# Kernel tuning notes

Measured on AMD Instinct MI355X. Metric: run time of the kernel, lower is better.

## Reference

```python
import jax, jax.numpy as jnp
import numpy as np

N = 50000      # nodes per graph
E = 600000     # edges per graph
IN_DIM = 512
HID = 128
LAYERS = 2


def setup_inputs() -> dict:
    key = jax.random.key(0)
    ks = jax.random.split(key, 24)
    s = 0.05
    inp = {
        "src_fea": jax.random.normal(ks[0], (N, IN_DIM), jnp.float32),
        "trg_fea": jax.random.normal(ks[1], (N, IN_DIM), jnp.float32),
        "src_row": jax.random.randint(ks[2], (E,), 0, N, jnp.int32),
        "src_col": jax.random.randint(ks[3], (E,), 0, N, jnp.int32),
        "trg_row": jax.random.randint(ks[4], (E,), 0, N, jnp.int32),
        "trg_col": jax.random.randint(ks[5], (E,), 0, N, jnp.int32),
        # fx: Linear(in,hid)+GELU+Linear(hid,hid)+GELU
        "fxW1": jax.random.normal(ks[6], (IN_DIM, HID), jnp.float32) * s,
        "fxb1": jnp.zeros((HID,), jnp.float32),
        "fxW2": jax.random.normal(ks[7], (HID, HID), jnp.float32) * s,
        "fxb2": jnp.zeros((HID,), jnp.float32),
        # edge_att_mlp: Linear(2h,20)+ReLU+Linear(20,10)+ReLU+Linear(10,1)+ReLU
        "eaW1": jax.random.normal(ks[8], (2 * HID, 20), jnp.float32) * s,
        "eab1": jnp.zeros((20,), jnp.float32),
        "eaW2": jax.random.normal(ks[9], (20, 10), jnp.float32) * s,
        "eab2": jnp.zeros((10,), jnp.float32),
        "eaW3": jax.random.normal(ks[10], (10, 1), jnp.float32) * s,
        "eab3": jnp.zeros((1,), jnp.float32),
        # GraphConv (PyG-style, bias=False): out = x@Wroot + agg@Wrel
        "convWroot": jax.random.normal(ks[11], (LAYERS, HID, HID), jnp.float32) * s,
        "convWrel": jax.random.normal(ks[12], (LAYERS, HID, HID), jnp.float32) * s,
    }
    return inp


def _fx(x, W1, b1, W2, b2):
    h = jax.nn.gelu(x @ W1 + b1, approximate=False)
    return jax.nn.gelu(h @ W2 + b2, approximate=False)


def _edge_att(e, eaW1, eab1, eaW2, eab2, eaW3, eab3):
    h = jax.nn.relu(e @ eaW1 + eab1)
    h = jax.nn.relu(h @ eaW2 + eab2)
    h = jax.nn.relu(h @ eaW3 + eab3)
    return jax.nn.sigmoid(h)  # [E,1]


def _graph_conv(x, row, col, ew, Wroot, Wrel):
    # message from source (row) gathered, weighted, aggregated at target (col)
    msg = ew[:, None] * x[row]                                  # [E,h]
    agg = jax.ops.segment_sum(msg, col, num_segments=N)         # [N,h]
    return x @ Wroot + agg @ Wrel


def _branch(x0, row, col, convWroot, convWrel, eaW1, eab1, eaW2, eab2, eaW3, eab3, hard):
    xs, cfds = [], []
    x = x0
    for i in range(LAYERS):
        edge_rep = jnp.concatenate([x[row], x[col]], axis=-1)    # [E,2h]
        att = _edge_att(edge_rep, eaW1, eab1, eaW2, eab2, eaW3, eab3)[:, 0]
        wc = (att + hard) * 0.5
        wo = 1.0 - wc
        x = jax.nn.soft_sign(_graph_conv(x, row, col, wc, convWroot[i], convWrel[i]))
        cfd = jax.nn.soft_sign(_graph_conv(x, row, col, wo, convWroot[i], convWrel[i]))
        xs.append(x)
        cfds.append(cfd)
    return xs, cfds


def reference(src_fea, trg_fea, src_row, src_col, trg_row, trg_col,
              fxW1, fxb1, fxW2, fxb2,
              eaW1, eab1, eaW2, eab2, eaW3, eab3,
              convWroot, convWrel):
    src1 = _fx(src_fea, fxW1, fxb1, fxW2, fxb2)
    trg1 = _fx(trg_fea, fxW1, fxb1, fxW2, fxb2)
    ea = (eaW1, eab1, eaW2, eab2, eaW3, eab3)
    xs_s, cf_s = _branch(src1, src_row, src_col, convWroot, convWrel, *ea, 0.0)
    xs_t, cf_t = _branch(trg1, trg_row, trg_col, convWroot, convWrel, *ea, 0.0)
    # stack: [src1, xs_s..., trg1, xs_t..., cf_s..., cf_t...] -> [2+2*LAYERS+2*LAYERS? no: 10, N, h]
    return jnp.stack([src1] + xs_s + [trg1] + xs_t + cf_s + cf_t, axis=0)
```

## Files before the change

### kernel.cpp

```cpp
#include <hip/hip_runtime.h>
#include <math.h>
#include <stdint.h>


typedef __attribute__((ext_vector_type(8))) short bh8;
typedef __attribute__((ext_vector_type(4))) float f4;

__device__ __forceinline__ float relu_f(float x) { return x > 0.f ? x : 0.f; }

__device__ __forceinline__ unsigned short f2bf(float f) {
    union { float f; unsigned u; } v; v.f = f;
    unsigned r = v.u + 0x7FFF + ((v.u >> 16) & 1);
    return (unsigned short)(r >> 16);
}
__device__ __forceinline__ float bf2f(unsigned short b) {
    union { unsigned u; float f; } v; v.u = ((unsigned)b) << 16;
    return v.f;
}

template<int ACT>
__device__ __forceinline__ float act_fn(float x) {
    if (ACT == 1) return 0.5f * x * (1.f + erff(x * 0.70710678118654752f));
    if (ACT == 2) return x / (1.f + fabsf(x));
    return x;
}

__device__ __forceinline__ float edge_att_mlp(const unsigned short* p1,
                                              const unsigned short* p2,
                                              const float* w2, const float* b2s,
                                              const float* w3s, const float* sb1,
                                              float sb3)
{
    bh8 a0 = *(const bh8*)&p1[0];
    bh8 a1 = *(const bh8*)&p1[8];
    ushort4 a2 = *(const ushort4*)&p1[16];
    bh8 b0 = *(const bh8*)&p2[0];
    bh8 b1 = *(const bh8*)&p2[8];
    ushort4 b2 = *(const ushort4*)&p2[16];

    float h1[20];
    #pragma unroll
    for (int j = 0; j < 8; ++j)
        h1[j] = relu_f(bf2f((unsigned short)a0[j]) + bf2f((unsigned short)b0[j]) + sb1[j]);
    #pragma unroll
    for (int j = 0; j < 8; ++j)
        h1[8 + j] = relu_f(bf2f((unsigned short)a1[j]) + bf2f((unsigned short)b1[j]) + sb1[8 + j]);
    h1[16] = relu_f(bf2f(a2.x) + bf2f(b2.x) + sb1[16]);
    h1[17] = relu_f(bf2f(a2.y) + bf2f(b2.y) + sb1[17]);
    h1[18] = relu_f(bf2f(a2.z) + bf2f(b2.z) + sb1[18]);
    h1[19] = relu_f(bf2f(a2.w) + bf2f(b2.w) + sb1[19]);

    float h3 = sb3;
    #pragma unroll
    for (int j2 = 0; j2 < 10; ++j2) {
        float s = b2s[j2];
        #pragma unroll
        for (int j = 0; j < 20; ++j)
            s = fmaf(h1[j], w2[j * 10 + j2], s);
        h3 = fmaf(relu_f(s), w3s[j2], h3);
    }
    h3 = relu_f(h3);
    return 1.f / (1.f + expf(-h3));
}

__device__ __forceinline__ void emit_p_phase(short* As, short* Bs,
                                             const short* __restrict__ W56,
                                             short* __restrict__ P,
                                             int row0, int M, int t)
{
    #pragma unroll
    for (int p = 0; p < 4; ++p) {
        int idx = t + 256 * p;
        int r = idx >> 4;
        int c = (idx & 15) * 8;
        *(bh8*)&Bs[r * 136 + c] = *(const bh8*)(W56 + r * 128 + c);
    }
    __syncthreads();
    const int lane = t & 63, w = t >> 6, l15 = lane & 15, l4 = lane >> 4;
    f4 accP[4];
    #pragma unroll
    for (int ni = 0; ni < 4; ++ni) accP[ni] = (f4){0.f, 0.f, 0.f, 0.f};
    #pragma unroll
    for (int kk = 0; kk < 4; ++kk) {
        bh8 a = *(const bh8*)&As[(w * 16 + l15) * 136 + kk * 32 + l4 * 8];
        #pragma unroll
        for (int ni = 0; ni < 4; ++ni) {
            bh8 b = *(const bh8*)&Bs[(ni * 16 + l15) * 136 + kk * 32 + l4 * 8];
            accP[ni] = __builtin_amdgcn_mfma_f32_16x16x32_bf16(a, b, accP[ni], 0, 0, 0);
        }
    }
    #pragma unroll
    for (int ni = 0; ni < 4; ++ni) {
        int col = ni * 16 + l15;
        #pragma unroll
        for (int r = 0; r < 4; ++r) {
            int row = row0 + w * 16 + l4 * 4 + r;
            if (row < M) P[(size_t)row * 64 + col] = (short)f2bf(accP[ni][r]);
        }
    }
}

template<int K, int AF, int ACT, bool BIAS, bool WF32, bool WB16, bool EMITP>
__global__ __launch_bounds__(256, 2)
void mfma_gemm(const void* __restrict__ X0a, const void* __restrict__ X0b,
               const short* __restrict__ W0t, const float* __restrict__ bias,
               float* __restrict__ outfA, short* __restrict__ outbA,
               float* __restrict__ outfB, short* __restrict__ outbB,
               const short* __restrict__ W56,
               short* __restrict__ PA, short* __restrict__ PB, int M)
{
    constexpr int BK  = 64;
    constexpr int LDA = EMITP ? 136 : 72;
    __shared__ short As[64 * LDA];
    __shared__ short Bs[128 * 72];

    const int half = gridDim.x >> 1;
    int bid = blockIdx.x;
    const int g1 = bid >= half;
    bid -= g1 ? half : 0;
    const void* X0v = g1 ? X0b : X0a;
    float* outf = g1 ? outfB : outfA;
    short* outb = g1 ? outbB : outbA;
    short* P    = g1 ? PB : PA;

    const int t    = threadIdx.x;
    const int row0 = bid * 64;
    const int lane = t & 63;
    const int w    = t >> 6;
    const int wr   = w & 1;
    const int wc   = w >> 1;
    const int l15  = lane & 15;
    const int l4   = lane >> 4;

    f4 acc[2][4];
    #pragma unroll
    for (int i = 0; i < 2; ++i)
        #pragma unroll
        for (int j = 0; j < 4; ++j)
            acc[i][j] = (f4){0.f, 0.f, 0.f, 0.f};

    const int ar = t >> 3;
    const int ac = (t & 7) * 8;

    #pragma unroll 1
    for (int k0 = 0; k0 < K; k0 += BK) {
        __syncthreads();
        #pragma unroll
        for (int p = 0; p < 2; ++p) {
            int r    = ar + p * 32;
            int grow = row0 + r;
            bh8 sv = {0, 0, 0, 0, 0, 0, 0, 0};
            if (AF == 0) {
                if (grow < M) {
                    const float* src = (const float*)X0v + (size_t)grow * K + k0 + ac;
                    float4 v0 = *(const float4*)src;
                    float4 v1 = *(const float4*)(src + 4);
                    sv[0] = (short)f2bf(v0.x); sv[1] = (short)f2bf(v0.y);
                    sv[2] = (short)f2bf(v0.z); sv[3] = (short)f2bf(v0.w);
                    sv[4] = (short)f2bf(v1.x); sv[5] = (short)f2bf(v1.y);
                    sv[6] = (short)f2bf(v1.z); sv[7] = (short)f2bf(v1.w);
                }
            } else {
                if (grow < M)
                    sv = *(const bh8*)((const short*)X0v + (size_t)grow * K + k0 + ac);
            }
            *(bh8*)&As[r * LDA + ac] = sv;
        }
        #pragma unroll
        for (int p = 0; p < 4; ++p) {
            int r = ar + p * 32;
            *(bh8*)&Bs[r * 72 + ac] = *(const bh8*)(W0t + (size_t)r * K + k0 + ac);
        }
        __syncthreads();
        #pragma unroll
        for (int kk = 0; kk < 2; ++kk) {
            bh8 a[2], b[4];
            #pragma unroll
            for (int mi = 0; mi < 2; ++mi)
                a[mi] = *(const bh8*)&As[(wr*32 + mi*16 + l15) * LDA + kk*32 + l4*8];
            #pragma unroll
            for (int ni = 0; ni < 4; ++ni)
                b[ni] = *(const bh8*)&Bs[(wc*64 + ni*16 + l15) * 72 + kk*32 + l4*8];
            #pragma unroll
            for (int mi = 0; mi < 2; ++mi)
                #pragma unroll
                for (int ni = 0; ni < 4; ++ni)
                    acc[mi][ni] = __builtin_amdgcn_mfma_f32_16x16x32_bf16(
                        a[mi], b[ni], acc[mi][ni], 0, 0, 0);
        }
    }

    if (EMITP) __syncthreads();
    #pragma unroll
    for (int mi = 0; mi < 2; ++mi) {
        #pragma unroll
        for (int ni = 0; ni < 4; ++ni) {
            int col = wc * 64 + ni * 16 + l15;
            float bv = BIAS ? bias[col] : 0.f;
            #pragma unroll
            for (int r = 0; r < 4; ++r) {
                int rloc = wr * 32 + mi * 16 + l4 * 4 + r;
                int row  = row0 + rloc;
                float v = act_fn<ACT>(acc[mi][ni][r] + bv);
                unsigned short bb = f2bf(v);
                if (row < M) {
                    if (WF32) outf[(size_t)row * 128 + col] = v;
                    if (WB16) outb[(size_t)row * 128 + col] = (short)bb;
                }
                if (EMITP) As[rloc * LDA + col] = (short)bb;
            }
        }
    }
    if (EMITP) emit_p_phase(As, Bs, W56, P, row0, M, t);
}

template<int MODE, bool WB16, bool EMITP, bool DOATT>
__global__ __launch_bounds__(256, 2)
void conv_fused(const short* __restrict__ XbA, const short* __restrict__ XbB,
                const int* __restrict__ coffA, const int* __restrict__ coffB,
                const int* __restrict__ crowA, const int* __restrict__ crowB,
                const float* __restrict__ attcA, const float* __restrict__ attcB,
                const short* __restrict__ Wroot, const short* __restrict__ Wrel,
                const short* __restrict__ W56,
                float* __restrict__ outfA, float* __restrict__ outfB,
                short* __restrict__ outbA, short* __restrict__ outbB,
                short* __restrict__ PA, short* __restrict__ PB,
                int convBlocks,
                const int* __restrict__ rowS, const int* __restrict__ colS,
                const int* __restrict__ rowT, const int* __restrict__ colT,
                const int* __restrict__ eposS, const int* __restrict__ eposT,
                const short* __restrict__ PinS, const short* __restrict__ PinT,
                const float* __restrict__ eab1, const float* __restrict__ eaW2,
                const float* __restrict__ eab2, const float* __restrict__ eaW3,
                const float* __restrict__ eab3,
                float* __restrict__ attOutS, float* __restrict__ attOutT,
                int E, int M)
{
    constexpr int LDA = 136;
    __shared__ short As[64 * LDA];
    __shared__ short Bs[128 * 72];

    const int t = threadIdx.x;

    if (DOATT && (int)blockIdx.x >= convBlocks) {
        float* ea = (float*)As;
        if (t < 200)       ea[t] = eaW2[t];
        else if (t < 210)  ea[t] = eab2[t - 200];
        else if (t < 220)  ea[t] = eaW3[t - 210];
        else if (t < 240)  ea[t] = eab1[t - 220];
        else if (t == 240) ea[240] = eab3[0];
        __syncthreads();
        int idx = ((int)blockIdx.x - convBlocks) * 256 + t;
        if (idx < 2 * E) {
            const int g1 = idx >= E;
            const int e  = idx - (g1 ? E : 0);
            const int* row  = g1 ? rowT  : rowS;
            const int* col  = g1 ? colT  : colS;
            const int* epos = g1 ? eposT : eposS;
            const short* P  = g1 ? PinT  : PinS;
            float* attOut   = g1 ? attOutT : attOutS;
            int r = row[e], c = col[e];
            const unsigned short* p1 = (const unsigned short*)P + (size_t)r * 64;
            const unsigned short* p2 = (const unsigned short*)P + (size_t)c * 64 + 32;
            attOut[epos[e]] = edge_att_mlp(p1, p2, ea, ea + 200, ea + 210, ea + 220, ea[240]);
        }
        return;
    }

    const int half = convBlocks >> 1;
    int bid = blockIdx.x;
    const int g1 = bid >= half;
    bid -= g1 ? half : 0;
    const short* Xb   = g1 ? XbB   : XbA;
    const int*   coff = g1 ? coffB : coffA;
    const int*   crow = g1 ? crowB : crowA;
    const float* attc = g1 ? attcB : attcA;
    float* outf = g1 ? outfB : outfA;
    short* outb = g1 ? outbB : outbA;
    short* P    = g1 ? PB : PA;

    const int row0 = bid * 64;
    const int lane = t & 63;
    const int w    = t >> 6;
    const int wr   = w & 1;
    const int wc   = w >> 1;
    const int l15  = lane & 15;
    const int l4   = lane >> 4;

    {
        const int g  = t >> 4;
        const int li = t & 15;
        #pragma unroll 1
        for (int q = 0; q < 4; ++q) {
            int rloc = g * 4 + q;
            int n = row0 + rloc;
            float a8[8] = {0.f, 0.f, 0.f, 0.f, 0.f, 0.f, 0.f, 0.f};
            if (n < M) {
                int p  = coff[n];
                int pe = coff[n + 1];
                for (; p + 7 < pe; p += 8) {
                    float w0 = attc[p],     w1 = attc[p + 1];
                    float w2 = attc[p + 2], w3 = attc[p + 3];
                    float w4 = attc[p + 4], w5 = attc[p + 5];
                    float w6 = attc[p + 6], w7 = attc[p + 7];
                    int r0 = crow[p],     r1 = crow[p + 1];
                    int r2 = crow[p + 2], r3 = crow[p + 3];
                    int r4 = crow[p + 4], r5 = crow[p + 5];
                    int r6 = crow[p + 6], r7 = crow[p + 7];
                    w0 = MODE ? fmaf(-0.5f, w0, 1.f) : 0.5f * w0;
                    w1 = MODE ? fmaf(-0.5f, w1, 1.f) : 0.5f * w1;
                    w2 = MODE ? fmaf(-0.5f, w2, 1.f) : 0.5f * w2;
                    w3 = MODE ? fmaf(-0.5f, w3, 1.f) : 0.5f * w3;
                    w4 = MODE ? fmaf(-0.5f, w4, 1.f) : 0.5f * w4;
                    w5 = MODE ? fmaf(-0.5f, w5, 1.f) : 0.5f * w5;
                    w6 = MODE ? fmaf(-0.5f, w6, 1.f) : 0.5f * w6;
                    w7 = MODE ? fmaf(-0.5f, w7, 1.f) : 0.5f * w7;
                    bh8 v0 = *(const bh8*)&Xb[(size_t)r0 * 128 + li * 8];
                    bh8 v1 = *(const bh8*)&Xb[(size_t)r1 * 128 + li * 8];
                    bh8 v2 = *(const bh8*)&Xb[(size_t)r2 * 128 + li * 8];
                    bh8 v3 = *(const bh8*)&Xb[(size_t)r3 * 128 + li * 8];
                    bh8 v4 = *(const bh8*)&Xb[(size_t)r4 * 128 + li * 8];
                    bh8 v5 = *(const bh8*)&Xb[(size_t)r5 * 128 + li * 8];
                    bh8 v6 = *(const bh8*)&Xb[(size_t)r6 * 128 + li * 8];
                    bh8 v7 = *(const bh8*)&Xb[(size_t)r7 * 128 + li * 8];
                    #pragma unroll
                    for (int j = 0; j < 8; ++j) {
                        a8[j] = fmaf(w0, bf2f((unsigned short)v0[j]), a8[j]);
                        a8[j] = fmaf(w1, bf2f((unsigned short)v1[j]), a8[j]);
                        a8[j] = fmaf(w2, bf2f((unsigned short)v2[j]), a8[j]);
                        a8[j] = fmaf(w3, bf2f((unsigned short)v3[j]), a8[j]);
                        a8[j] = fmaf(w4, bf2f((unsigned short)v4[j]), a8[j]);
                        a8[j] = fmaf(w5, bf2f((unsigned short)v5[j]), a8[j]);
                        a8[j] = fmaf(w6, bf2f((unsigned short)v6[j]), a8[j]);
                        a8[j] = fmaf(w7, bf2f((unsigned short)v7[j]), a8[j]);
                    }
                }
                for (; p + 3 < pe; p += 4) {
                    float w0 = attc[p],     w1 = attc[p + 1];
                    float w2 = attc[p + 2], w3 = attc[p + 3];
                    int r0 = crow[p],     r1 = crow[p + 1];
                    int r2 = crow[p + 2], r3 = crow[p + 3];
                    w0 = MODE ? fmaf(-0.5f, w0, 1.f) : 0.5f * w0;
                    w1 = MODE ? fmaf(-0.5f, w1, 1.f) : 0.5f * w1;
                    w2 = MODE ? fmaf(-0.5f, w2, 1.f) : 0.5f * w2;
                    w3 = MODE ? fmaf(-0.5f, w3, 1.f) : 0.5f * w3;
                    bh8 v0 = *(const bh8*)&Xb[(size_t)r0 * 128 + li * 8];
                    bh8 v1 = *(const bh8*)&Xb[(size_t)r1 * 128 + li * 8];
                    bh8 v2 = *(const bh8*)&Xb[(size_t)r2 * 128 + li * 8];
                    bh8 v3 = *(const bh8*)&Xb[(size_t)r3 * 128 + li * 8];
                    #pragma unroll
                    for (int j = 0; j < 8; ++j) {
                        a8[j] = fmaf(w0, bf2f((unsigned short)v0[j]), a8[j]);
                        a8[j] = fmaf(w1, bf2f((unsigned short)v1[j]), a8[j]);
                        a8[j] = fmaf(w2, bf2f((unsigned short)v2[j]), a8[j]);
                        a8[j] = fmaf(w3, bf2f((unsigned short)v3[j]), a8[j]);
                    }
                }
                for (; p < pe; ++p) {
                    float w0 = attc[p];
                    int   r0 = crow[p];
                    w0 = MODE ? fmaf(-0.5f, w0, 1.f) : 0.5f * w0;
                    bh8 v0 = *(const bh8*)&Xb[(size_t)r0 * 128 + li * 8];
                    #pragma unroll
                    for (int j = 0; j < 8; ++j)
                        a8[j] = fmaf(w0, bf2f((unsigned short)v0[j]), a8[j]);
                }
            }
            bh8 o;
            #pragma unroll
            for (int j = 0; j < 8; ++j) o[j] = (short)f2bf(a8[j]);
            *(bh8*)&As[rloc * LDA + li * 8] = o;
        }
    }
    __syncthreads();

    f4 acc[2][4];
    #pragma unroll
    for (int i = 0; i < 2; ++i)
        #pragma unroll
        for (int j = 0; j < 4; ++j)
            acc[i][j] = (f4){0.f, 0.f, 0.f, 0.f};

    const int ar = t >> 3;
    const int ac = (t & 7) * 8;

    #pragma unroll 1
    for (int k0 = 0; k0 < 128; k0 += 64) {
        if (k0) __syncthreads();
        #pragma unroll
        for (int p = 0; p < 4; ++p) {
            int r = ar + p * 32;
            *(bh8*)&Bs[r * 72 + ac] = *(const bh8*)(Wrel + (size_t)r * 128 + k0 + ac);
        }
        __syncthreads();
        #pragma unroll
        for (int kk = 0; kk < 2; ++kk) {
            bh8 a[2], b[4];
            #pragma unroll
            for (int mi = 0; mi < 2; ++mi)
                a[mi] = *(const bh8*)&As[(wr*32 + mi*16 + l15) * LDA + k0 + kk*32 + l4*8];
            #pragma unroll
            for (int ni = 0; ni < 4; ++ni)
                b[ni] = *(const bh8*)&Bs[(wc*64 + ni*16 + l15) * 72 + kk*32 + l4*8];
            #pragma unroll
            for (int mi = 0; mi < 2; ++mi)
                #pragma unroll
                for (int ni = 0; ni < 4; ++ni)
                    acc[mi][ni] = __builtin_amdgcn_mfma_f32_16x16x32_bf16(
                        a[mi], b[ni], acc[mi][ni], 0, 0, 0);
        }
    }

    #pragma unroll 1
    for (int k0 = 0; k0 < 128; k0 += 64) {
        __syncthreads();
        #pragma unroll
        for (int p = 0; p < 2; ++p) {
            int r    = ar + p * 32;
            int grow = row0 + r;
            bh8 sv = {0, 0, 0, 0, 0, 0, 0, 0};
            if (grow < M)
                sv = *(const bh8*)(Xb + (size_t)grow * 128 + k0 + ac);
            *(bh8*)&As[r * LDA + ac] = sv;
        }
        #pragma unroll
        for (int p = 0; p < 4; ++p) {
            int r = ar + p * 32;
            *(bh8*)&Bs[r * 72 + ac] = *(const bh8*)(Wroot + (size_t)r * 128 + k0 + ac);
        }
        __syncthreads();
        #pragma unroll
        for (int kk = 0; kk < 2; ++kk) {
            bh8 a[2], b[4];
            #pragma unroll
            for (int mi = 0; mi < 2; ++mi)
                a[mi] = *(const bh8*)&As[(wr*32 + mi*16 + l15) * LDA + kk*32 + l4*8];
            #pragma unroll
            for (int ni = 0; ni < 4; ++ni)
                b[ni] = *(const bh8*)&Bs[(wc*64 + ni*16 + l15) * 72 + kk*32 + l4*8];
            #pragma unroll
            for (int mi = 0; mi < 2; ++mi)
                #pragma unroll
                for (int ni = 0; ni < 4; ++ni)
                    acc[mi][ni] = __builtin_amdgcn_mfma_f32_16x16x32_bf16(
                        a[mi], b[ni], acc[mi][ni], 0, 0, 0);
        }
    }

    if (EMITP) __syncthreads();
    #pragma unroll
    for (int mi = 0; mi < 2; ++mi) {
        #pragma unroll
        for (int ni = 0; ni < 4; ++ni) {
            int col = wc * 64 + ni * 16 + l15;
            #pragma unroll
            for (int r = 0; r < 4; ++r) {
                int rloc = wr * 32 + mi * 16 + l4 * 4 + r;
                int row  = row0 + rloc;
                float v = act_fn<2>(acc[mi][ni][r]);
                unsigned short bb = f2bf(v);
                if (row < M) {
                    outf[(size_t)row * 128 + col] = v;
                    if (WB16) outb[(size_t)row * 128 + col] = (short)bb;
                }
                if (EMITP) As[rloc * LDA + col] = (short)bb;
            }
        }
    }
    if (EMITP) emit_p_phase(As, Bs, W56, P, row0, M, t);
}

__global__ void prep_hist(const float* __restrict__ eaW1, const float* __restrict__ fxW1,
                          const float* __restrict__ fxW2, const float* __restrict__ convWroot,
                          const float* __restrict__ convWrel,
                          short* __restrict__ w56, short* __restrict__ fxW1t,
                          short* __restrict__ fxW2t, short* __restrict__ wrt,
                          short* __restrict__ wlt,
                          const int* __restrict__ colS, const int* __restrict__ colT,
                          int* __restrict__ deg, int N, int E, int prepBlocks)
{
    if ((int)blockIdx.x >= prepBlocks) {
        int idx = (blockIdx.x - prepBlocks) * 256 + threadIdx.x;
        if (idx >= 2 * E) return;
        const int g1 = idx >= E;
        const int e  = idx - (g1 ? E : 0);
        int c = (g1 ? colT : colS)[e];
        atomicAdd(&deg[(size_t)g1 * N + c], 1);
        return;
    }
    int i = blockIdx.x * 256 + threadIdx.x;
    if (i < 64 * 128) {
        int j = i >> 7, k = i & 127;
        float v = 0.f;
        if (j < 20)                  v = eaW1[k * 20 + j];
        else if (j >= 32 && j < 52)  v = eaW1[(128 + k) * 20 + (j - 32)];
        w56[i] = (short)f2bf(v);
        return;
    }
    i -= 64 * 128;
    if (i < 512 * 128) {
        int k = i >> 7, n = i & 127;
        fxW1t[(size_t)n * 512 + k] = (short)f2bf(fxW1[i]);
        return;
    }
    i -= 512 * 128;
    if (i < 128 * 128) {
        int k = i >> 7, n = i & 127;
        fxW2t[n * 128 + k] = (short)f2bf(fxW2[i]);
        return;
    }
    i -= 128 * 128;
    if (i < 2 * 128 * 128) {
        int L = i >> 14, r = i & 16383;
        int k = r >> 7, n = r & 127;
        wrt[L * 16384 + n * 128 + k] = (short)f2bf(convWroot[i]);
        return;
    }
    i -= 2 * 128 * 128;
    if (i < 2 * 128 * 128) {
        int L = i >> 14, r = i & 16383;
        int k = r >> 7, n = r & 127;
        wlt[L * 16384 + n * 128 + k] = (short)f2bf(convWrel[i]);
    }
}

__device__ __forceinline__ int block_incl_scan(int v, int* wsum)
{
    int lane = threadIdx.x & 63;
    int w    = threadIdx.x >> 6;
    #pragma unroll
    for (int off = 1; off < 64; off <<= 1) {
        int t = __shfl_up(v, off);
        if (lane >= off) v += t;
    }
    if (lane == 63) wsum[w] = v;
    __syncthreads();
    int add = 0;
    for (int j = 0; j < w; ++j) add += wsum[j];
    return v + add;
}

__global__ __launch_bounds__(256)
void scanA_both(const int* __restrict__ deg, int* __restrict__ coffS,
                int* __restrict__ coffT, int* __restrict__ bsum, int N)
{
    __shared__ int wsum[4];
    int gy = blockIdx.y;
    const int* d = deg + (size_t)gy * N;
    int* coff    = gy ? coffT : coffS;
    int* bs      = bsum + gy * 256;
    int i = blockIdx.x * 256 + threadIdx.x;
    int orig = (i < N) ? d[i] : 0;
    int v = block_incl_scan(orig, wsum);
    if (i < N) coff[i] = v - orig;
    if (threadIdx.x == 255) bs[blockIdx.x] = v;
}

__global__ __launch_bounds__(256)
void scanB_both(const int* __restrict__ bsum, int* __restrict__ boff, int nb)
{
    __shared__ int wsum[4];
    int gy = blockIdx.y;
    const int* bs = bsum + gy * 256;
    int* bo       = boff + gy * 256;
    int tid = threadIdx.x;
    int orig = (tid < nb) ? bs[tid] : 0;
    int v = block_incl_scan(orig, wsum);
    if (tid < nb) bo[tid] = v - orig;
}

__global__ __launch_bounds__(256)
void scanC_both(int* __restrict__ coffS, int* __restrict__ coffT,
                const int* __restrict__ boff, int* __restrict__ curS,
                int* __restrict__ curT, int N, int E)
{
    int gy = blockIdx.y;
    int* coff = gy ? coffT : coffS;
    int* cur  = gy ? curT  : curS;
    const int* bo = boff + gy * 256;
    int i = blockIdx.x * 256 + threadIdx.x;
    if (i < N) {
        int v = coff[i] + bo[i >> 8];
        coff[i] = v;
        cur[i]  = v;
    }
    if (i == 0) coff[N] = E;
}

__global__ __launch_bounds__(256)
void fill_att_both(const int* __restrict__ rowS, const int* __restrict__ colS,
                   const int* __restrict__ rowT, const int* __restrict__ colT,
                   int* __restrict__ curS, int* __restrict__ curT,
                   int* __restrict__ crowS, int* __restrict__ crowT,
                   int* __restrict__ eposS, int* __restrict__ eposT,
                   const short* __restrict__ PS, const short* __restrict__ PT,
                   const float* __restrict__ eab1, const float* __restrict__ eaW2,
                   const float* __restrict__ eab2, const float* __restrict__ eaW3,
                   const float* __restrict__ eab3,
                   float* __restrict__ attcS, float* __restrict__ attcT, int E)
{
    __shared__ float w2[200], b2s[10], w3s[10], sb1[20], sb3;
    int t = threadIdx.x;
    if (t < 200) w2[t] = eaW2[t];
    if (t < 20)  sb1[t] = eab1[t];
    if (t < 10)  { b2s[t] = eab2[t]; w3s[t] = eaW3[t]; }
    if (t == 0)  sb3 = eab3[0];
    __syncthreads();

    int idx = blockIdx.x * 256 + t;
    if (idx >= 2 * E) return;
    const int g1 = idx >= E;
    const int e  = idx - (g1 ? E : 0);
    const int* row = g1 ? rowT : rowS;
    const int* col = g1 ? colT : colS;
    int* cur  = g1 ? curT  : curS;
    int* crow = g1 ? crowT : crowS;
    int* epos = g1 ? eposT : eposS;
    const short* P = g1 ? PT : PS;
    float* attc    = g1 ? attcT : attcS;

    int c = col[e];
    int r = row[e];
    int p = atomicAdd(&cur[c], 1);
    crow[p] = r;
    epos[e] = p;

    const unsigned short* p1 = (const unsigned short*)P + (size_t)r * 64;
    const unsigned short* p2 = (const unsigned short*)P + (size_t)c * 64 + 32;
    attc[p] = edge_att_mlp(p1, p2, w2, b2s, w3s, sb1, sb3);
}


extern "C" void kernel_launch(void* const* d_in, const int* in_sizes, int n_in,
                              void* d_out, int out_size, void* d_ws, size_t ws_size,
                              hipStream_t stream)
{
    const float* src_fea = (const float*)d_in[0];
    const float* trg_fea = (const float*)d_in[1];
    const int*   src_row = (const int*)d_in[2];
    const int*   src_col = (const int*)d_in[3];
    const int*   trg_row = (const int*)d_in[4];
    const int*   trg_col = (const int*)d_in[5];
    const float* fxW1 = (const float*)d_in[6];
    const float* fxb1 = (const float*)d_in[7];
    const float* fxW2 = (const float*)d_in[8];
    const float* fxb2 = (const float*)d_in[9];
    const float* eaW1 = (const float*)d_in[10];
    const float* eab1 = (const float*)d_in[11];
    const float* eaW2 = (const float*)d_in[12];
    const float* eab2 = (const float*)d_in[13];
    const float* eaW3 = (const float*)d_in[14];
    const float* eab3 = (const float*)d_in[15];
    const float* convWroot = (const float*)d_in[16];
    const float* convWrel  = (const float*)d_in[17];

    const int N = in_sizes[0] / 512;
    const int E = in_sizes[2];

    float* out = (float*)d_out;
    const size_t slot_sz = (size_t)N * 128;
    auto slot = [&](int i) { return out + (size_t)i * slot_sz; };

    float* fp     = (float*)d_ws;
    float* attcS0 = fp; fp += E;
    float* attcT0 = fp; fp += E;
    float* attcS1 = fp; fp += E;
    float* attcT1 = fp; fp += E;
    int* ip    = (int*)fp;
    int* deg   = ip; ip += 2 * N;
    int* bsum  = ip; ip += 512;
    int* boff  = ip; ip += 512;
    int* coffS = ip; ip += N + 2;
    int* coffT = ip; ip += N + 2;
    int* curS  = ip; ip += N;
    int* curT  = ip; ip += N;
    int* crowS = ip; ip += E;
    int* crowT = ip; ip += E;
    int* eposS = ip; ip += E;
    int* eposT = ip; ip += E;
    short* sp = (short*)((((uintptr_t)ip) + 255) & ~(uintptr_t)255);
    short* xb0   = sp; sp += slot_sz;
    short* xb1   = sp; sp += slot_sz;
    short* xsbS[2]; short* xsbT[2];
    xsbS[0] = sp; sp += slot_sz;
    xsbS[1] = sp; sp += slot_sz;
    xsbT[0] = sp; sp += slot_sz;
    xsbT[1] = sp; sp += slot_sz;
    short* PS    = sp; sp += (size_t)N * 64;
    short* PT    = sp; sp += (size_t)N * 64;
    short* w56   = sp; sp += 64 * 128;
    short* fxW1t = sp; sp += 128 * 512;
    short* fxW2t = sp; sp += 128 * 128;
    short* wrt   = sp; sp += 2 * 128 * 128;
    short* wlt   = sp; sp += 2 * 128 * 128;

    const int e2grid  = (2 * E + 255) / 256;
    const int nchunks = (N + 255) / 256;

    hipMemsetAsync(deg, 0, (size_t)2 * N * sizeof(int), stream);
    const int prep_total = 64*128 + 512*128 + 128*128 + 2*128*128 + 2*128*128;
    const int prepBlocks = (prep_total + 255) / 256;
    prep_hist<<<prepBlocks + e2grid, 256, 0, stream>>>(
        eaW1, fxW1, fxW2, convWroot, convWrel, w56, fxW1t, fxW2t, wrt, wlt,
        src_col, trg_col, deg, N, E, prepBlocks);

    const int gb = (N + 63) / 64;
    short* hS = xsbS[0];
    short* hT = xsbT[0];
    mfma_gemm<512, 0, 1, true, false, true, false><<<2 * gb, 256, 0, stream>>>(
        src_fea, trg_fea, fxW1t, fxb1,
        nullptr, hS, nullptr, hT, nullptr, nullptr, nullptr, N);
    mfma_gemm<128, 1, 1, true, true, true, true><<<2 * gb, 256, 0, stream>>>(
        hS, hT, fxW2t, fxb2,
        slot(0), xb0, slot(3), xb1, w56, PS, PT, N);

    scanA_both<<<dim3(nchunks, 2), 256, 0, stream>>>(deg, coffS, coffT, bsum, N);
    scanB_both<<<dim3(1, 2), 256, 0, stream>>>(bsum, boff, nchunks);
    scanC_both<<<dim3(nchunks, 2), 256, 0, stream>>>(coffS, coffT, boff, curS, curT, N, E);
    fill_att_both<<<e2grid, 256, 0, stream>>>(
        src_row, src_col, trg_row, trg_col, curS, curT, crowS, crowT,
        eposS, eposT, PS, PT, eab1, eaW2, eab2, eaW3, eab3, attcS0, attcT0, E);

    const short* WrT0 = wrt;
    const short* WlT0 = wlt;
    const short* WrT1 = wrt + 16384;
    const short* WlT1 = wlt + 16384;

    conv_fused<0, true, true, false><<<2 * gb, 256, 0, stream>>>(
        xb0, xb1, coffS, coffT, crowS, crowT, attcS0, attcT0,
        WrT0, WlT0, w56, slot(1), slot(4), xsbS[0], xsbT[0], PS, PT,
        2 * gb, nullptr, nullptr, nullptr, nullptr, nullptr, nullptr,
        nullptr, nullptr, nullptr, nullptr, nullptr, nullptr, nullptr,
        nullptr, nullptr, E, N);

    conv_fused<1, false, false, true><<<2 * gb + e2grid, 256, 0, stream>>>(
        xsbS[0], xsbT[0], coffS, coffT, crowS, crowT, attcS0, attcT0,
        WrT0, WlT0, nullptr, slot(6), slot(8), nullptr, nullptr, nullptr, nullptr,
        2 * gb, src_row, src_col, trg_row, trg_col, eposS, eposT,
        PS, PT, eab1, eaW2, eab2, eaW3, eab3, attcS1, attcT1, E, N);

    conv_fused<0, true, false, false><<<2 * gb, 256, 0, stream>>>(
        xsbS[0], xsbT[0], coffS, coffT, crowS, crowT, attcS1, attcT1,
        WrT1, WlT1, nullptr, slot(2), slot(5), xsbS[1], xsbT[1], nullptr, nullptr,
        2 * gb, nullptr, nullptr, nullptr, nullptr, nullptr, nullptr,
        nullptr, nullptr, nullptr, nullptr, nullptr, nullptr, nullptr,
        nullptr, nullptr, E, N);

    conv_fused<1, false, false, false><<<2 * gb, 256, 0, stream>>>(
        xsbS[1], xsbT[1], coffS, coffT, crowS, crowT, attcS1, attcT1,
        WrT1, WlT1, nullptr, slot(7), slot(9), nullptr, nullptr, nullptr, nullptr,
        2 * gb, nullptr, nullptr, nullptr, nullptr, nullptr, nullptr,
        nullptr, nullptr, nullptr, nullptr, nullptr, nullptr, nullptr,
        nullptr, nullptr, E, N);
}
```

Before: 590.2 us.

## Split neighbor aggregation out of fused conv kernel into standalone gather kernel

The CSR gather-and-weight aggregation that used to run inside the MFMA conv kernel (64 rows per block, 2 blocks/CU launch bound) now runs in a separate lightweight kernel with one 16-lane group per node. It writes a bf16 aggregate buffer, which the conv kernel then loads into shared memory. The intent is higher occupancy and better latency hiding for the irregular gathers, which were limited by the GEMM kernel's LDS and register footprint. In exchange it adds four kernel launches and an extra write and read of an N×128 bf16 buffer per conv.

```diff
diff --git a/kernel.cpp b/kernel.cpp
--- a/kernel.cpp
+++ b/kernel.cpp
@@ -214,27 +214,120 @@
     if (EMITP) emit_p_phase(As, Bs, W56, P, row0, M, t);
 }
 
-template<int MODE, bool WB16, bool EMITP, bool DOATT>
+template<int MODE>
+__global__ __launch_bounds__(256)
+void agg_kern(const short* __restrict__ XbA, const short* __restrict__ XbB,
+              const int* __restrict__ coffA, const int* __restrict__ coffB,
+              const int* __restrict__ crowA, const int* __restrict__ crowB,
+              const float* __restrict__ attcA, const float* __restrict__ attcB,
+              short* __restrict__ aggA, short* __restrict__ aggB, int N)
+{
+    int ng = blockIdx.x * 16 + (threadIdx.x >> 4);
+    if (ng >= 2 * N) return;
+    const int g1 = ng >= N;
+    const int n  = ng - (g1 ? N : 0);
+    const short* Xb   = g1 ? XbB   : XbA;
+    const int*   coff = g1 ? coffB : coffA;
+    const int*   crow = g1 ? crowB : crowA;
+    const float* attc = g1 ? attcB : attcA;
+    short*       aggb = g1 ? aggB  : aggA;
+    const int li = threadIdx.x & 15;
+
+    float a8[8] = {0.f, 0.f, 0.f, 0.f, 0.f, 0.f, 0.f, 0.f};
+    int p  = coff[n];
+    int pe = coff[n + 1];
+    for (; p + 7 < pe; p += 8) {
+        float w0 = attc[p],     w1 = attc[p + 1];
+        float w2 = attc[p + 2], w3 = attc[p + 3];
+        float w4 = attc[p + 4], w5 = attc[p + 5];
+        float w6 = attc[p + 6], w7 = attc[p + 7];
+        int r0 = crow[p],     r1 = crow[p + 1];
+        int r2 = crow[p + 2], r3 = crow[p + 3];
+        int r4 = crow[p + 4], r5 = crow[p + 5];
+        int r6 = crow[p + 6], r7 = crow[p + 7];
+        w0 = MODE ? fmaf(-0.5f, w0, 1.f) : 0.5f * w0;
+        w1 = MODE ? fmaf(-0.5f, w1, 1.f) : 0.5f * w1;
+        w2 = MODE ? fmaf(-0.5f, w2, 1.f) : 0.5f * w2;
+        w3 = MODE ? fmaf(-0.5f, w3, 1.f) : 0.5f * w3;
+        w4 = MODE ? fmaf(-0.5f, w4, 1.f) : 0.5f * w4;
+        w5 = MODE ? fmaf(-0.5f, w5, 1.f) : 0.5f * w5;
+        w6 = MODE ? fmaf(-0.5f, w6, 1.f) : 0.5f * w6;
+        w7 = MODE ? fmaf(-0.5f, w7, 1.f) : 0.5f * w7;
+        bh8 v0 = *(const bh8*)&Xb[(size_t)r0 * 128 + li * 8];
+        bh8 v1 = *(const bh8*)&Xb[(size_t)r1 * 128 + li * 8];
+        bh8 v2 = *(const bh8*)&Xb[(size_t)r2 * 128 + li * 8];
+        bh8 v3 = *(const bh8*)&Xb[(size_t)r3 * 128 + li * 8];
+        bh8 v4 = *(const bh8*)&Xb[(size_t)r4 * 128 + li * 8];
+        bh8 v5 = *(const bh8*)&Xb[(size_t)r5 * 128 + li * 8];
+        bh8 v6 = *(const bh8*)&Xb[(size_t)r6 * 128 + li * 8];
+        bh8 v7 = *(const bh8*)&Xb[(size_t)r7 * 128 + li * 8];
+        #pragma unroll
+        for (int j = 0; j < 8; ++j) {
+            a8[j] = fmaf(w0, bf2f((unsigned short)v0[j]), a8[j]);
+            a8[j] = fmaf(w1, bf2f((unsigned short)v1[j]), a8[j]);
+            a8[j] = fmaf(w2, bf2f((unsigned short)v2[j]), a8[j]);
+            a8[j] = fmaf(w3, bf2f((unsigned short)v3[j]), a8[j]);
+            a8[j] = fmaf(w4, bf2f((unsigned short)v4[j]), a8[j]);
+            a8[j] = fmaf(w5, bf2f((unsigned short)v5[j]), a8[j]);
+            a8[j] = fmaf(w6, bf2f((unsigned short)v6[j]), a8[j]);
+            a8[j] = fmaf(w7, bf2f((unsigned short)v7[j]), a8[j]);
+        }
+    }
+    for (; p + 3 < pe; p += 4) {
+        float w0 = attc[p],     w1 = attc[p + 1];
+        float w2 = attc[p + 2], w3 = attc[p + 3];
+        int r0 = crow[p],     r1 = crow[p + 1];
+        int r2 = crow[p + 2], r3 = crow[p + 3];
+        w0 = MODE ? fmaf(-0.5f, w0, 1.f) : 0.5f * w0;
+        w1 = MODE ? fmaf(-0.5f, w1, 1.f) : 0.5f * w1;
+        w2 = MODE ? fmaf(-0.5f, w2, 1.f) : 0.5f * w2;
+        w3 = MODE ? fmaf(-0.5f, w3, 1.f) : 0.5f * w3;
+        bh8 v0 = *(const bh8*)&Xb[(size_t)r0 * 128 + li * 8];
+        bh8 v1 = *(const bh8*)&Xb[(size_t)r1 * 128 + li * 8];
+        bh8 v2 = *(const bh8*)&Xb[(size_t)r2 * 128 + li * 8];
+        bh8 v3 = *(const bh8*)&Xb[(size_t)r3 * 128 + li * 8];
+        #pragma unroll
+        for (int j = 0; j < 8; ++j) {
+            a8[j] = fmaf(w0, bf2f((unsigned short)v0[j]), a8[j]);
+            a8[j] = fmaf(w1, bf2f((unsigned short)v1[j]), a8[j]);
+            a8[j] = fmaf(w2, bf2f((unsigned short)v2[j]), a8[j]);
+            a8[j] = fmaf(w3, bf2f((unsigned short)v3[j]), a8[j]);
+        }
+    }
+    for (; p < pe; ++p) {
+        float w0 = attc[p];
+        int   r0 = crow[p];
+        w0 = MODE ? fmaf(-0.5f, w0, 1.f) : 0.5f * w0;
+        bh8 v0 = *(const bh8*)&Xb[(size_t)r0 * 128 + li * 8];
+        #pragma unroll
+        for (int j = 0; j < 8; ++j)
+            a8[j] = fmaf(w0, bf2f((unsigned short)v0[j]), a8[j]);
+    }
+    bh8 o;
+    #pragma unroll
+    for (int j = 0; j < 8; ++j) o[j] = (short)f2bf(a8[j]);
+    *(bh8*)&aggb[(size_t)n * 128 + li * 8] = o;
+}
+
+template<bool WB16, bool EMITP, bool DOATT>
 __global__ __launch_bounds__(256, 2)
-void conv_fused(const short* __restrict__ XbA, const short* __restrict__ XbB,
-                const int* __restrict__ coffA, const int* __restrict__ coffB,
-                const int* __restrict__ crowA, const int* __restrict__ crowB,
-                const float* __restrict__ attcA, const float* __restrict__ attcB,
-                const short* __restrict__ Wroot, const short* __restrict__ Wrel,
-                const short* __restrict__ W56,
-                float* __restrict__ outfA, float* __restrict__ outfB,
-                short* __restrict__ outbA, short* __restrict__ outbB,
-                short* __restrict__ PA, short* __restrict__ PB,
-                int convBlocks,
-                const int* __restrict__ rowS, const int* __restrict__ colS,
-                const int* __restrict__ rowT, const int* __restrict__ colT,
-                const int* __restrict__ eposS, const int* __restrict__ eposT,
-                const short* __restrict__ PinS, const short* __restrict__ PinT,
-                const float* __restrict__ eab1, const float* __restrict__ eaW2,
-                const float* __restrict__ eab2, const float* __restrict__ eaW3,
-                const float* __restrict__ eab3,
-                float* __restrict__ attOutS, float* __restrict__ attOutT,
-                int E, int M)
+void conv_ns(const short* __restrict__ XbA, const short* __restrict__ XbB,
+             const short* __restrict__ aggA, const short* __restrict__ aggB,
+             const short* __restrict__ Wroot, const short* __restrict__ Wrel,
+             const short* __restrict__ W56,
+             float* __restrict__ outfA, float* __restrict__ outfB,
+             short* __restrict__ outbA, short* __restrict__ outbB,
+             short* __restrict__ PA, short* __restrict__ PB,
+             int convBlocks,
+             const int* __restrict__ rowS, const int* __restrict__ colS,
+             const int* __restrict__ rowT, const int* __restrict__ colT,
+             const int* __restrict__ eposS, const int* __restrict__ eposT,
+             const short* __restrict__ PinS, const short* __restrict__ PinT,
+             const float* __restrict__ eab1, const float* __restrict__ eaW2,
+             const float* __restrict__ eab2, const float* __restrict__ eaW3,
+             const float* __restrict__ eab3,
+             float* __restrict__ attOutS, float* __restrict__ attOutT,
+             int E, int M)
 {
     constexpr int LDA = 136;
     __shared__ short As[64 * LDA];
@@ -271,10 +364,8 @@
     int bid = blockIdx.x;
     const int g1 = bid >= half;
     bid -= g1 ? half : 0;
-    const short* Xb   = g1 ? XbB   : XbA;
-    const int*   coff = g1 ? coffB : coffA;
-    const int*   crow = g1 ? crowB : crowA;
-    const float* attc = g1 ? attcB : attcA;
+    const short* Xb   = g1 ? XbB  : XbA;
+    const short* aggb = g1 ? aggB : aggA;
     float* outf = g1 ? outfB : outfA;
     short* outb = g1 ? outbB : outbA;
     short* P    = g1 ? PB : PA;
@@ -288,88 +379,16 @@
     const int l4   = lane >> 4;
 
     {
-        const int g  = t >> 4;
-        const int li = t & 15;
-        #pragma unroll 1
-        for (int q = 0; q < 4; ++q) {
-            int rloc = g * 4 + q;
-            int n = row0 + rloc;
-            float a8[8] = {0.f, 0.f, 0.f, 0.f, 0.f, 0.f, 0.f, 0.f};
-            if (n < M) {
-                int p  = coff[n];
-                int pe = coff[n + 1];
-                for (; p + 7 < pe; p += 8) {
-                    float w0 = attc[p],     w1 = attc[p + 1];
-                    float w2 = attc[p + 2], w3 = attc[p + 3];
-                    float w4 = attc[p + 4], w5 = attc[p + 5];
-                    float w6 = attc[p + 6], w7 = attc[p + 7];
-                    int r0 = crow[p],     r1 = crow[p + 1];
-                    int r2 = crow[p + 2], r3 = crow[p + 3];
-                    int r4 = crow[p + 4], r5 = crow[p + 5];
-                    int r6 = crow[p + 6], r7 = crow[p + 7];
-                    w0 = MODE ? fmaf(-0.5f, w0, 1.f) : 0.5f * w0;
-                    w1 = MODE ? fmaf(-0.5f, w1, 1.f) : 0.5f * w1;
-                    w2 = MODE ? fmaf(-0.5f, w2, 1.f) : 0.5f * w2;
-                    w3 = MODE ? fmaf(-0.5f, w3, 1.f) : 0.5f * w3;
-                    w4 = MODE ? fmaf(-0.5f, w4, 1.f) : 0.5f * w4;
-                    w5 = MODE ? fmaf(-0.5f, w5, 1.f) : 0.5f * w5;
-                    w6 = MODE ? fmaf(-0.5f, w6, 1.f) : 0.5f * w6;
-                    w7 = MODE ? fmaf(-0.5f, w7, 1.f) : 0.5f * w7;
-                    bh8 v0 = *(const bh8*)&Xb[(size_t)r0 * 128 + li * 8];
-                    bh8 v1 = *(const bh8*)&Xb[(size_t)r1 * 128 + li * 8];
-                    bh8 v2 = *(const bh8*)&Xb[(size_t)r2 * 128 + li * 8];
-                    bh8 v3 = *(const bh8*)&Xb[(size_t)r3 * 128 + li * 8];
-                    bh8 v4 = *(const bh8*)&Xb[(size_t)r4 * 128 + li * 8];
-                    bh8 v5 = *(const bh8*)&Xb[(size_t)r5 * 128 + li * 8];
-                    bh8 v6 = *(const bh8*)&Xb[(size_t)r6 * 128 + li * 8];
-                    bh8 v7 = *(const bh8*)&Xb[(size_t)r7 * 128 + li * 8];
-                    #pragma unroll
-                    for (int j = 0; j < 8; ++j) {
-                        a8[j] = fmaf(w0, bf2f((unsigned short)v0[j]), a8[j]);
-                        a8[j] = fmaf(w1, bf2f((unsigned short)v1[j]), a8[j]);
-                        a8[j] = fmaf(w2, bf2f((unsigned short)v2[j]), a8[j]);
-                        a8[j] = fmaf(w3, bf2f((unsigned short)v3[j]), a8[j]);
-                        a8[j] = fmaf(w4, bf2f((unsigned short)v4[j]), a8[j]);
-                        a8[j] = fmaf(w5, bf2f((unsigned short)v5[j]), a8[j]);
-                        a8[j] = fmaf(w6, bf2f((unsigned short)v6[j]), a8[j]);
-                        a8[j] = fmaf(w7, bf2f((unsigned short)v7[j]), a8[j]);
-                    }
-                }
-                for (; p + 3 < pe; p += 4) {
-                    float w0 = attc[p],     w1 = attc[p + 1];
-                    float w2 = attc[p + 2], w3 = attc[p + 3];
-                    int r0 = crow[p],     r1 = crow[p + 1];
-                    int r2 = crow[p + 2], r3 = crow[p + 3];
-                    w0 = MODE ? fmaf(-0.5f, w0, 1.f) : 0.5f * w0;
-                    w1 = MODE ? fmaf(-0.5f, w1, 1.f) : 0.5f * w1;
-                    w2 = MODE ? fmaf(-0.5f, w2, 1.f) : 0.5f * w2;
-                    w3 = MODE ? fmaf(-0.5f, w3, 1.f) : 0.5f * w3;
-                    bh8 v0 = *(const bh8*)&Xb[(size_t)r0 * 128 + li * 8];
-                    bh8 v1 = *(const bh8*)&Xb[(size_t)r1 * 128 + li * 8];
-                    bh8 v2 = *(const bh8*)&Xb[(size_t)r2 * 128 + li * 8];
-                    bh8 v3 = *(const bh8*)&Xb[(size_t)r3 * 128 + li * 8];
-                    #pragma unroll
-                    for (int j = 0; j < 8; ++j) {
-                        a8[j] = fmaf(w0, bf2f((unsigned short)v0[j]), a8[j]);
-                        a8[j] = fmaf(w1, bf2f((unsigned short)v1[j]), a8[j]);
-                        a8[j] = fmaf(w2, bf2f((unsigned short)v2[j]), a8[j]);
-                        a8[j] = fmaf(w3, bf2f((unsigned short)v3[j]), a8[j]);
-                    }
-                }
-                for (; p < pe; ++p) {
-                    float w0 = attc[p];
-                    int   r0 = crow[p];
-                    w0 = MODE ? fmaf(-0.5f, w0, 1.f) : 0.5f * w0;
-                    bh8 v0 = *(const bh8*)&Xb[(size_t)r0 * 128 + li * 8];
-                    #pragma unroll
-                    for (int j = 0; j < 8; ++j)
-                        a8[j] = fmaf(w0, bf2f((unsigned short)v0[j]), a8[j]);
-                }
-            }
-            bh8 o;
-            #pragma unroll
-            for (int j = 0; j < 8; ++j) o[j] = (short)f2bf(a8[j]);
-            *(bh8*)&As[rloc * LDA + li * 8] = o;
+        const int r0l = t >> 4;
+        const int c   = (t & 15) * 8;
+        #pragma unroll
+        for (int p = 0; p < 4; ++p) {
+            int r    = r0l + p * 16;
+            int grow = row0 + r;
+            bh8 sv = {0, 0, 0, 0, 0, 0, 0, 0};
+            if (grow < M)
+                sv = *(const bh8*)(aggb + (size_t)grow * 128 + c);
+            *(bh8*)&As[r * LDA + c] = sv;
         }
     }
     __syncthreads();
@@ -696,6 +715,7 @@
 
     const int e2grid  = (2 * E + 255) / 256;
     const int nchunks = (N + 255) / 256;
+    const int agrid   = (2 * N + 15) / 16;
 
     hipMemsetAsync(deg, 0, (size_t)2 * N * sizeof(int), stream);
     const int prep_total = 64*128 + 512*128 + 128*128 + 2*128*128 + 2*128*128;
@@ -726,29 +746,38 @@
     const short* WrT1 = wrt + 16384;
     const short* WlT1 = wlt + 16384;
 
-    conv_fused<0, true, true, false><<<2 * gb, 256, 0, stream>>>(
-        xb0, xb1, coffS, coffT, crowS, crowT, attcS0, attcT0,
-        WrT0, WlT0, w56, slot(1), slot(4), xsbS[0], xsbT[0], PS, PT,
+    short* aggS_a = xsbS[1]; short* aggT_a = xsbT[1];
+    short* aggS_b = xb0;     short* aggT_b = xb1;
+
+    agg_kern<0><<<agrid, 256, 0, stream>>>(xb0, xb1, coffS, coffT, crowS, crowT,
+                                           attcS0, attcT0, aggS_a, aggT_a, N);
+    conv_ns<true, true, false><<<2 * gb, 256, 0, stream>>>(
+        xb0, xb1, aggS_a, aggT_a, WrT0, WlT0, w56,
+        slot(1), slot(4), xsbS[0], xsbT[0], PS, PT,
         2 * gb, nullptr, nullptr, nullptr, nullptr, nullptr, nullptr,
         nullptr, nullptr, nullptr, nullptr, nullptr, nullptr, nullptr,
         nullptr, nullptr, E, N);
-
-    conv_fused<1, false, false, true><<<2 * gb + e2grid, 256, 0, stream>>>(
-        xsbS[0], xsbT[0], coffS, coffT, crowS, crowT, attcS0, attcT0,
-        WrT0, WlT0, nullptr, slot(6), slot(8), nullptr, nullptr, nullptr, nullptr,
+    agg_kern<1><<<agrid, 256, 0, stream>>>(xsbS[0], xsbT[0], coffS, coffT, crowS, crowT,
+                                           attcS0, attcT0, aggS_b, aggT_b, N);
+    conv_ns<false, false, true><<<2 * gb + e2grid, 256, 0, stream>>>(
+        xsbS[0], xsbT[0], aggS_b, aggT_b, WrT0, WlT0, nullptr,
+        slot(6), slot(8), nullptr, nullptr, nullptr, nullptr,
         2 * gb, src_row, src_col, trg_row, trg_col, eposS, eposT,
         PS, PT, eab1, eaW2, eab2, eaW3, eab3, attcS1, attcT1, E, N);
 
-    conv_fused<0, true, false, false><<<2 * gb, 256, 0, stream>>>(
-        xsbS[0], xsbT[0], coffS, coffT, crowS, crowT, attcS1, attcT1,
-        WrT1, WlT1, nullptr, slot(2), slot(5), xsbS[1], xsbT[1], nullptr, nullptr,
+    agg_kern<0><<<agrid, 256, 0, stream>>>(xsbS[0], xsbT[0], coffS, coffT, crowS, crowT,
+                                           attcS1, attcT1, aggS_b, aggT_b, N);
+    conv_ns<true, false, false><<<2 * gb, 256, 0, stream>>>(
+        xsbS[0], xsbT[0], aggS_b, aggT_b, WrT1, WlT1, nullptr,
+        slot(2), slot(5), xsbS[1], xsbT[1], nullptr, nullptr,
         2 * gb, nullptr, nullptr, nullptr, nullptr, nullptr, nullptr,
         nullptr, nullptr, nullptr, nullptr, nullptr, nullptr, nullptr,
         nullptr, nullptr, E, N);
-
-    conv_fused<1, false, false, false><<<2 * gb, 256, 0, stream>>>(
-        xsbS[1], xsbT[1], coffS, coffT, crowS, crowT, attcS1, attcT1,
-        WrT1, WlT1, nullptr, slot(7), slot(9), nullptr, nullptr, nullptr, nullptr,
+    agg_kern<1><<<agrid, 256, 0, stream>>>(xsbS[1], xsbT[1], coffS, coffT, crowS, crowT,
+                                           attcS1, attcT1, aggS_b, aggT_b, N);
+    conv_ns<false, false, false><<<2 * gb, 256, 0, stream>>>(
+        xsbS[1], xsbT[1], aggS_b, aggT_b, WrT1, WlT1, nullptr,
+        slot(7), slot(9), nullptr, nullptr, nullptr, nullptr,
         2 * gb, nullptr, nullptr, nullptr, nullptr, nullptr, nullptr,
         nullptr, nullptr, nullptr, nullptr, nullptr, nullptr, nullptr,
         nullptr, nullptr, E, N);
```

After: 619.3 us. 1.05x slower.
